# Performance work log

Measured on AMD Instinct MI355X. Metric: run time of the kernel, lower is better.

The kernel has to match this reference:

```python
import jax, jax.numpy as jnp
import numpy as np

EPS = 1e-6
SIGMA = 0.1  # temperature for pseudo-LBS blend weights


def _quat_rotate(q, v):
    # q: [..., 4] (w, x, y, z) unit quaternions, v: [..., 3]
    qw, qv = q[..., :1], q[..., 1:]
    t = 2.0 * jnp.cross(qv, v)
    return v + qw * t + jnp.cross(qv, t)


def _pairwise_sqdist(a, b):
    # a: [n, d], b: [m, d] -> [n, m]
    return (jnp.sum(a * a, -1, keepdims=True)
            + jnp.sum(b * b, -1)[None, :]
            - 2.0 * (a @ b.T))


def setup_inputs() -> dict:
    N, K, F, V, J, P, M, H = 300000, 80, 64, 6890, 24, 64, 64, 128
    key = jax.random.key(0)
    ks = jax.random.split(key, 16)
    s = lambda i, shape: jax.random.normal(ks[i], shape, dtype=jnp.float32) * 0.05
    return {
        "xyz": jax.random.normal(ks[0], (N, 3), dtype=jnp.float32),
        "feature": jax.random.normal(ks[1], (N, F), dtype=jnp.float32),
        "centers": jax.random.normal(ks[2], (K, F), dtype=jnp.float32),
        "smpl_verts": jax.random.normal(ks[3], (V, 3), dtype=jnp.float32),
        "skinning_weights": jax.random.uniform(ks[4], (V, J), dtype=jnp.float32),
        "body_pose_feature": jax.random.normal(ks[5], (J, P), dtype=jnp.float32),
        "w_body": s(6, (P + F, M)),
        "b_body": jnp.zeros((M,), jnp.float32),
        "w_pos1": s(7, (3 + M, H)),
        "b_pos1": jnp.zeros((H,), jnp.float32),
        "w_pos2": s(8, (H, M)),
        "b_pos2": jnp.zeros((M,), jnp.float32),
        "w_rot": s(9, (M, 4)),
        "b_rot": jnp.zeros((4,), jnp.float32),
        "w_trans": s(10, (M, 3)),
        "b_trans": jnp.zeros((3,), jnp.float32),
    }


def reference(xyz, feature, centers, smpl_verts, skinning_weights,
              body_pose_feature, w_body, b_body, w_pos1, b_pos1,
              w_pos2, b_pos2, w_rot, b_rot, w_trans, b_trans):
    # ---- soft k-means: soft assignment of N points to K garment joints ----
    a = jax.nn.softmax(-_pairwise_sqdist(feature, centers), axis=-1)  # [N, K]
    cnt = a.sum(axis=0) + EPS                                          # [K]
    # weighted segment-reduce: c_assign^T @ xyz, diag(1/count) normalize
    joint_xyz = (a.T @ xyz) / cnt[:, None]      # [K, 3]
    joint_feat = (a.T @ feature) / cnt[:, None]  # [K, F] (cluster centers)

    # ---- KNN (k=1) skin-weight lookup against SMPL canonical verts ----
    idx = jnp.argmin(_pairwise_sqdist(joint_xyz, smpl_verts), axis=-1)  # [K]
    pts_W = skinning_weights[idx]                                        # [K, J]

    # ---- garment pose decoder ----
    body_feat = pts_W @ body_pose_feature                 # [K, P]
    g = jnp.concatenate([body_feat, joint_feat], axis=-1)  # [K, P+F]
    g = jax.nn.gelu(g @ w_body + b_body)                   # [K, M]
    lo, hi = smpl_verts.min(0), smpl_verts.max(0)
    xn = 2.0 * (joint_xyz - lo) / (hi - lo + EPS) - 1.0    # aabb sym-normalize
    h = jax.nn.relu(jnp.concatenate([xn, g], -1) @ w_pos1 + b_pos1)
    g2 = h @ w_pos2 + b_pos2                               # [K, M]
    q = g2 @ w_rot + b_rot
    q = q / (jnp.linalg.norm(q, axis=-1, keepdims=True) + EPS)  # [K, 4]
    t = g2 @ w_trans + b_trans                                   # [K, 3]

    # ---- pseudo-LBS: blend per-joint transforms back to N points ----
    w = jax.nn.softmax(-_pairwise_sqdist(xyz, joint_xyz) / SIGMA, axis=-1)  # [N, K]
    qb = w @ q
    qb = qb / (jnp.linalg.norm(qb, axis=-1, keepdims=True) + EPS)  # [N, 4]
    deformed_xyz = _quat_rotate(qb, xyz) + w @ t                    # [N, 3]
    return deformed_xyz
```

## Files before the change

### kernel.cpp

```cpp
#include <hip/hip_runtime.h>
#include <math.h>

#define N_PTS 300000
#define NJ 80
#define FDIM 64
#define VN 6890
#define NROUND 9375
#define GRID_A 256
#define TOTW 2048
#define SLOT_B 8704

typedef __attribute__((ext_vector_type(8))) short short8;
typedef __attribute__((ext_vector_type(4))) float f32x4;

union Frag { uint32_t u[4]; short8 v; };

__device__ __forceinline__ uint32_t packhi(float a, float b) {
  return (__float_as_uint(a) >> 16) | (__float_as_uint(b) & 0xFFFF0000u);
}
__device__ __forceinline__ uint32_t packlo(float a, float b) {
  float la = a - __uint_as_float(__float_as_uint(a) & 0xFFFF0000u);
  float lb = b - __uint_as_float(__float_as_uint(b) & 0xFFFF0000u);
  return packhi(la, lb);
}

#define DPPF(x, ctrl) __uint_as_float((uint32_t)__builtin_amdgcn_update_dpp( \
    0, (int)__float_as_uint(x), (ctrl), 0xF, 0xF, true))

__device__ __forceinline__ void gl16(const float* g, const void* l) {
  __builtin_amdgcn_global_load_lds(
      (const __attribute__((address_space(1))) void*)g,
      (__attribute__((address_space(3))) void*)l, 16, 0, 0);
}
__device__ __forceinline__ void gl4(const float* g, const void* l) {
  __builtin_amdgcn_global_load_lds(
      (const __attribute__((address_space(1))) void*)g,
      (__attribute__((address_space(3))) void*)l, 4, 0, 0);
}

__global__ __launch_bounds__(512, 2) void kA(
    const float* __restrict__ xyz, const float* __restrict__ feature,
    const float* __restrict__ centers, float* __restrict__ jacc,
    float* __restrict__ part)
{
  __shared__ __align__(16) unsigned char ring[8][2][SLOT_B];
  __shared__ ushort sChi[NJ][72];
  __shared__ ushort sClo[NJ][72];

  const int tid = threadIdx.x;
  const int w = tid >> 6;
  const int l = tid & 63;
  const int i = l & 15;
  const int g = l >> 4;
  const int gw = blockIdx.x * 8 + w;

  auto STAGE = [&](int st, int rs) {
    const float* fb = feature + (size_t)rs * 2048;
    unsigned char* base = &ring[w][st][0];
#pragma unroll
    for (int k = 0; k < 8; ++k) {
      const int lu = k * 64 + l;
      const int ptl = lu >> 4;
      const int gu = ptl * 16 + ((lu & 15) ^ (ptl & 7));
      gl16(fb + gu * 4, base + k * 1024);
    }
    const float* xb = xyz + (size_t)rs * 96;
#pragma unroll
    for (int k = 0; k < 2; ++k) {
      int fi = k * 64 + l; if (fi > 95) fi = 95;
      gl4(xb + fi, base + 8192 + k * 256);
    }
  };

  STAGE(0, gw);

  for (int idx = tid; idx < NJ * FDIM; idx += 512) {
    float f = centers[idx];
    sChi[idx >> 6][idx & 63] = (ushort)(__float_as_uint(f) >> 16);
    float lo = f - __uint_as_float(__float_as_uint(f) & 0xFFFF0000u);
    sClo[idx >> 6][idx & 63] = (ushort)(__float_as_uint(lo) >> 16);
  }
  float cn[5];
#pragma unroll
  for (int nt = 0; nt < 5; ++nt) {
    float s = 0.f;
    const float* cp = centers + (size_t)(i + 16 * nt) * FDIM + 8 * g;
#pragma unroll
    for (int e = 0; e < 8; ++e) {
      float a0 = cp[e], a1 = cp[32 + e];
      s += a0 * a0 + a1 * a1;
    }
    s += __shfl_xor(s, 16);
    s += __shfl_xor(s, 32);
    cn[nt] = s;
  }
  __syncthreads();

  f32x4 acc2[5][5];
#pragma unroll
  for (int a = 0; a < 5; ++a)
#pragma unroll
    for (int b = 0; b < 5; ++b) acc2[a][b] = (f32x4){0.f, 0.f, 0.f, 0.f};

  int s2 = 0;
  for (int r = gw; r < NROUND; r += TOTW) {
    {
      int rn = r + TOTW; if (rn > NROUND - 1) rn = NROUND - 1;
      STAGE(s2 ^ 1, rn);
    }
    asm volatile("s_waitcnt vmcnt(10)" ::: "memory");
    __builtin_amdgcn_sched_barrier(0);

    const float* F = (const float*)&ring[w][s2][0];
    const float* X = (const float*)&ring[w][s2][8192];

    f32x4 acc1[2][5];
#pragma unroll
    for (int c = 0; c < 2; ++c)
#pragma unroll
      for (int nt = 0; nt < 5; ++nt) acc1[c][nt] = (f32x4){0.f, 0.f, 0.f, 0.f};

#pragma unroll
    for (int ks = 0; ks < 2; ++ks) {
      Frag ah[2], al[2];
#pragma unroll
      for (int c = 0; c < 2; ++c) {
        const int ptl = 16 * c + i;
        const int m = ptl & 7;
        const int j = 8 * ks + 2 * g;
        float4 va = *(const float4*)(F + ptl * 64 + ((j ^ m) << 2));
        float4 vb = *(const float4*)(F + ptl * 64 + (((j + 1) ^ m) << 2));
        ah[c].u[0] = packhi(va.x, va.y); ah[c].u[1] = packhi(va.z, va.w);
        ah[c].u[2] = packhi(vb.x, vb.y); ah[c].u[3] = packhi(vb.z, vb.w);
        al[c].u[0] = packlo(va.x, va.y); al[c].u[1] = packlo(va.z, va.w);
        al[c].u[2] = packlo(vb.x, vb.y); al[c].u[3] = packlo(vb.z, vb.w);
      }
#pragma unroll
      for (int nt = 0; nt < 5; ++nt) {
        Frag bh, bl;
        *(uint4*)bh.u = *(const uint4*)&sChi[i + 16 * nt][32 * ks + 8 * g];
        *(uint4*)bl.u = *(const uint4*)&sClo[i + 16 * nt][32 * ks + 8 * g];
#pragma unroll
        for (int c = 0; c < 2; ++c) {
          acc1[c][nt] = __builtin_amdgcn_mfma_f32_16x16x32_bf16(ah[c].v, bh.v, acc1[c][nt], 0, 0, 0);
          acc1[c][nt] = __builtin_amdgcn_mfma_f32_16x16x32_bf16(al[c].v, bh.v, acc1[c][nt], 0, 0, 0);
          acc1[c][nt] = __builtin_amdgcn_mfma_f32_16x16x32_bf16(ah[c].v, bl.v, acc1[c][nt], 0, 0, 0);
        }
      }
    }

    Frag pA[5];
#pragma unroll
    for (int c = 0; c < 2; ++c) {
      f32x4 e5[5];
#pragma unroll
      for (int nt = 0; nt < 5; ++nt)
#pragma unroll
        for (int rr = 0; rr < 4; ++rr) e5[nt][rr] = 2.f * acc1[c][nt][rr] - cn[nt];
      float rs[4];
#pragma unroll
      for (int rr = 0; rr < 4; ++rr) {
        float mm = e5[0][rr];
#pragma unroll
        for (int nt = 1; nt < 5; ++nt) mm = fmaxf(mm, e5[nt][rr]);
        mm = fmaxf(mm, DPPF(mm, 0xB1));
        mm = fmaxf(mm, DPPF(mm, 0x4E));
        mm = fmaxf(mm, DPPF(mm, 0x141));
        mm = fmaxf(mm, DPPF(mm, 0x140));
        float ss = 0.f;
#pragma unroll
        for (int nt = 0; nt < 5; ++nt) {
          float e = __expf(e5[nt][rr] - mm);
          e5[nt][rr] = e;
          ss += e;
        }
        ss += DPPF(ss, 0xB1);
        ss += DPPF(ss, 0x4E);
        ss += DPPF(ss, 0x141);
        ss += DPPF(ss, 0x140);
        rs[rr] = __builtin_amdgcn_rcpf(ss);
      }
#pragma unroll
      for (int nt = 0; nt < 5; ++nt) {
        pA[nt].u[2 * c + 0] = packhi(e5[nt][0] * rs[0], e5[nt][1] * rs[1]);
        pA[nt].u[2 * c + 1] = packhi(e5[nt][2] * rs[2], e5[nt][3] * rs[3]);
      }
    }

#pragma unroll
    for (int ct = 0; ct < 5; ++ct) {
      Frag B;
      float x[8];
      if (ct < 4) {
        const int d = 16 * ct + i, jd = d >> 2, db = d & 3;
#pragma unroll
        for (int n = 0; n < 8; ++n) {
          const int ptl = (n < 4) ? (4 * g + n) : (16 + 4 * g + (n - 4));
          x[n] = F[ptl * 64 + ((jd ^ (ptl & 7)) << 2) + db];
        }
      } else {
#pragma unroll
        for (int n = 0; n < 8; ++n) {
          const int ptl = (n < 4) ? (4 * g + n) : (16 + 4 * g + (n - 4));
          x[n] = (i < 3) ? X[ptl * 3 + i] : (i == 3 ? 1.f : 0.f);
        }
      }
      B.u[0] = packhi(x[0], x[1]); B.u[1] = packhi(x[2], x[3]);
      B.u[2] = packhi(x[4], x[5]); B.u[3] = packhi(x[6], x[7]);
#pragma unroll
      for (int nt = 0; nt < 5; ++nt)
        acc2[nt][ct] = __builtin_amdgcn_mfma_f32_16x16x32_bf16(pA[nt].v, B.v, acc2[nt][ct], 0, 0, 0);
    }

    s2 ^= 1;
  }

  asm volatile("s_waitcnt vmcnt(0)" ::: "memory");
  __syncthreads();
  float* sJ = (float*)&ring[0][0][0];
  for (int idx = tid; idx < 5440; idx += 512) sJ[idx] = 0.f;
  __syncthreads();
#pragma unroll
  for (int ww = 0; ww < 8; ++ww) {
    if (w == ww) {
#pragma unroll
      for (int nt = 0; nt < 5; ++nt)
#pragma unroll
        for (int ct = 0; ct < 5; ++ct) {
          if (ct < 4 || i < 4) {
            const int col = 16 * ct + i;
#pragma unroll
            for (int rr = 0; rr < 4; ++rr)
              sJ[(16 * nt + 4 * g + rr) * 68 + col] += acc2[nt][ct][rr];
          }
        }
    }
    __syncthreads();
  }
  if (part) {
    for (int idx = tid; idx < 5440; idx += 512)
      part[(size_t)blockIdx.x * 5440 + idx] = sJ[idx];
  } else {
    for (int idx = tid; idx < 5440; idx += 512)
      atomicAdd(&jacc[idx], sJ[idx]);
  }
}

__global__ __launch_bounds__(64) void kB(
    const float* __restrict__ jacc, const float* __restrict__ part,
    const float* __restrict__ smpl,
    const float* __restrict__ sw, const float* __restrict__ bpf,
    const float* __restrict__ w_body, const float* __restrict__ b_body,
    const float* __restrict__ w_pos1, const float* __restrict__ b_pos1,
    const float* __restrict__ w_pos2, const float* __restrict__ b_pos2,
    const float* __restrict__ w_rot,  const float* __restrict__ b_rot,
    const float* __restrict__ w_trans,const float* __restrict__ b_trans,
    float* __restrict__ jpack, float* __restrict__ qpack,
    float* __restrict__ tpack)
{
  const int k = blockIdx.x;
  const int l = threadIdx.x;
  __shared__ float sh68[68];
  __shared__ float gin[128];
  __shared__ float in2[67];
  __shared__ float h2[128];
  __shared__ float g2[64];
  __shared__ float q7[8];

  if (part) {
    float a0 = 0.f, a1 = 0.f, a2 = 0.f, a3 = 0.f;
    float e0 = 0.f, e1 = 0.f, e2 = 0.f, e3 = 0.f;
    const float* pk = part + k * 68;
    for (int b = 0; b < GRID_A; b += 4) {
      a0 += pk[(size_t)(b + 0) * 5440 + l];
      a1 += pk[(size_t)(b + 1) * 5440 + l];
      a2 += pk[(size_t)(b + 2) * 5440 + l];
      a3 += pk[(size_t)(b + 3) * 5440 + l];
      if (l < 4) {
        e0 += pk[(size_t)(b + 0) * 5440 + 64 + l];
        e1 += pk[(size_t)(b + 1) * 5440 + 64 + l];
        e2 += pk[(size_t)(b + 2) * 5440 + 64 + l];
        e3 += pk[(size_t)(b + 3) * 5440 + 64 + l];
      }
    }
    sh68[l] = (a0 + a1) + (a2 + a3);
    if (l < 4) sh68[64 + l] = (e0 + e1) + (e2 + e3);
  } else {
    sh68[l] = jacc[k * 68 + l];
    if (l < 4) sh68[64 + l] = jacc[k * 68 + 64 + l];
  }
  __syncthreads();

  const float cnt = sh68[67] + 1e-6f;
  gin[64 + l] = sh68[l] / cnt;
  const float jx = sh68[64] / cnt;
  const float jy = sh68[65] / cnt;
  const float jz = sh68[66] / cnt;

  float lo0 = 1e30f, lo1 = 1e30f, lo2 = 1e30f;
  float hi0 = -1e30f, hi1 = -1e30f, hi2 = -1e30f;
  float best = 1e30f; int bi = 0;
  for (int v = l; v < VN; v += 64) {
    float x = smpl[v*3], y = smpl[v*3+1], z = smpl[v*3+2];
    lo0 = fminf(lo0, x); hi0 = fmaxf(hi0, x);
    lo1 = fminf(lo1, y); hi1 = fmaxf(hi1, y);
    lo2 = fminf(lo2, z); hi2 = fmaxf(hi2, z);
    float dx = x - jx, dy = y - jy, dz = z - jz;
    float d = dx*dx + dy*dy + dz*dz;
    if (d < best) { best = d; bi = v; }
  }
#pragma unroll
  for (int m = 1; m < 64; m <<= 1) {
    lo0 = fminf(lo0, __shfl_xor(lo0, m));
    lo1 = fminf(lo1, __shfl_xor(lo1, m));
    lo2 = fminf(lo2, __shfl_xor(lo2, m));
    hi0 = fmaxf(hi0, __shfl_xor(hi0, m));
    hi1 = fmaxf(hi1, __shfl_xor(hi1, m));
    hi2 = fmaxf(hi2, __shfl_xor(hi2, m));
    float d2 = __shfl_xor(best, m); int i2 = __shfl_xor(bi, m);
    if (d2 < best || (d2 == best && i2 < bi)) { best = d2; bi = i2; }
  }

  {
    float s = 0.f;
    for (int j = 0; j < 24; ++j) s += sw[bi*24 + j] * bpf[j*64 + l];
    gin[l] = s;
  }
  if (l < 3) {
    float lo = (l == 0) ? lo0 : (l == 1) ? lo1 : lo2;
    float hi = (l == 0) ? hi0 : (l == 1) ? hi1 : hi2;
    float jc = (l == 0) ? jx : (l == 1) ? jy : jz;
    in2[l] = 2.f * (jc - lo) / (hi - lo + 1e-6f) - 1.f;
  }
  __syncthreads();

  {
    float s = b_body[l];
    for (int t = 0; t < 128; ++t) s += gin[t] * w_body[t*64 + l];
    float u = 0.7978845608028654f * (s + 0.044715f * s * s * s);
    float e = __expf(2.f * u);
    float th = 1.f - 2.f / (e + 1.f);
    in2[3 + l] = 0.5f * s * (1.f + th);
  }
  __syncthreads();

#pragma unroll
  for (int half = 0; half < 2; ++half) {
    const int m = l + 64*half;
    float s = b_pos1[m];
    for (int t = 0; t < 67; ++t) s += in2[t] * w_pos1[t*128 + m];
    h2[m] = fmaxf(s, 0.f);
  }
  __syncthreads();

  {
    float s = b_pos2[l];
    for (int t = 0; t < 128; ++t) s += h2[t] * w_pos2[t*64 + l];
    g2[l] = s;
  }
  __syncthreads();

  if (l < 4) {
    float s = b_rot[l];
    for (int t = 0; t < 64; ++t) s += g2[t] * w_rot[t*4 + l];
    q7[l] = s;
  } else if (l < 7) {
    const int j = l - 4;
    float s = b_trans[j];
    for (int t = 0; t < 64; ++t) s += g2[t] * w_trans[t*3 + j];
    q7[l] = s;
  }
  __syncthreads();
  if (l == 0) {
    float q0 = q7[0], q1 = q7[1], q2 = q7[2], q3 = q7[3];
    float rn = 1.f / (sqrtf(q0*q0 + q1*q1 + q2*q2 + q3*q3) + 1e-6f);
    *(float4*)&qpack[k*4] = make_float4(q0*rn, q1*rn, q2*rn, q3*rn);
    *(float4*)&tpack[k*4] = make_float4(q7[4], q7[5], q7[6], 0.f);
    *(float4*)&jpack[k*4] = make_float4(jx, jy, jz, jx*jx + jy*jy + jz*jz);
  }
}

__global__ __launch_bounds__(256) void kC(
    const float* __restrict__ xyz, const float* __restrict__ jpack,
    const float* __restrict__ qpack, const float* __restrict__ tpack,
    float* __restrict__ out)
{
  __shared__ float4 sj[NJ], sq[NJ], st[NJ];
  __shared__ float sxy[768];
  const int tid = threadIdx.x;
  const int pbase = blockIdx.x * 256;
  const int nval = min(256, N_PTS - pbase);
  const int cnt3 = nval * 3;

  if (tid < 80)        sj[tid]       = ((const float4*)jpack)[tid];
  else if (tid < 160)  sq[tid - 80]  = ((const float4*)qpack)[tid - 80];
  else if (tid < 240)  st[tid - 160] = ((const float4*)tpack)[tid - 160];
  for (int t = tid; t < cnt3; t += 256) sxy[t] = xyz[(size_t)pbase * 3 + t];
  __syncthreads();

  const bool valid = tid < nval;
  float x0 = 0.f, x1 = 0.f, x2 = 0.f;
  if (valid) { x0 = sxy[tid*3]; x1 = sxy[tid*3+1]; x2 = sxy[tid*3+2]; }
  __syncthreads();

  float lv[NJ];
  float m = -1e30f;
#pragma unroll
  for (int k = 0; k < NJ; ++k) {
    float4 j = sj[k];
    lv[k] = (2.f*(x0*j.x + x1*j.y + x2*j.z) - j.w) * 10.0f;
    m = fmaxf(m, lv[k]);
  }
  float s = 0.f;
  float qb0=0,qb1=0,qb2=0,qb3=0, tb0=0,tb1=0,tb2=0;
#pragma unroll
  for (int k = 0; k < NJ; ++k) {
    float e = __expf(lv[k] - m);
    s += e;
    float4 q = sq[k];
    float4 t = st[k];
    qb0 += e*q.x; qb1 += e*q.y; qb2 += e*q.z; qb3 += e*q.w;
    tb0 += e*t.x; tb1 += e*t.y; tb2 += e*t.z;
  }
  float rs = 1.f / s;
  qb0*=rs; qb1*=rs; qb2*=rs; qb3*=rs; tb0*=rs; tb1*=rs; tb2*=rs;
  float nrm = sqrtf(qb0*qb0+qb1*qb1+qb2*qb2+qb3*qb3) + 1e-6f;
  float rn = 1.f / nrm;
  float qw = qb0*rn, qx = qb1*rn, qy = qb2*rn, qz = qb3*rn;
  float t2x = 2.f*(qy*x2 - qz*x1);
  float t2y = 2.f*(qz*x0 - qx*x2);
  float t2z = 2.f*(qx*x1 - qy*x0);
  float cx = qy*t2z - qz*t2y;
  float cy = qz*t2x - qx*t2z;
  float cz = qx*t2y - qy*t2x;
  float r0 = x0 + qw*t2x + cx + tb0;
  float r1 = x1 + qw*t2y + cy + tb1;
  float r2 = x2 + qw*t2z + cz + tb2;

  if (valid) { sxy[tid*3] = r0; sxy[tid*3+1] = r1; sxy[tid*3+2] = r2; }
  __syncthreads();
  for (int t = tid; t < cnt3; t += 256) out[(size_t)pbase * 3 + t] = sxy[t];
}

extern "C" void kernel_launch(void* const* d_in, const int* in_sizes, int n_in,
                              void* d_out, int out_size, void* d_ws, size_t ws_size,
                              hipStream_t stream) {
  const float* xyz     = (const float*)d_in[0];
  const float* feature = (const float*)d_in[1];
  const float* centers = (const float*)d_in[2];
  const float* smpl    = (const float*)d_in[3];
  const float* sw      = (const float*)d_in[4];
  const float* bpf     = (const float*)d_in[5];
  const float* w_body  = (const float*)d_in[6];
  const float* b_body  = (const float*)d_in[7];
  const float* w_pos1  = (const float*)d_in[8];
  const float* b_pos1  = (const float*)d_in[9];
  const float* w_pos2  = (const float*)d_in[10];
  const float* b_pos2  = (const float*)d_in[11];
  const float* w_rot   = (const float*)d_in[12];
  const float* b_rot   = (const float*)d_in[13];
  const float* w_trans = (const float*)d_in[14];
  const float* b_trans = (const float*)d_in[15];
  float* out = (float*)d_out;

  float* ws    = (float*)d_ws;
  float* jacc  = ws;
  float* jpack = ws + 5440;
  float* qpack = ws + 5760;
  float* tpack = ws + 6080;
  float* part  = ws + 6400;

  const size_t need = (size_t)6400 + (size_t)GRID_A * 5440;
  const bool use_part = (ws_size / 4) >= need;
  float* part_arg = use_part ? part : nullptr;

  if (!use_part) hipMemsetAsync(jacc, 0, 5440 * sizeof(float), stream);
  kA<<<dim3(GRID_A), dim3(512), 0, stream>>>(xyz, feature, centers, jacc, part_arg);
  kB<<<dim3(NJ), dim3(64), 0, stream>>>(jacc, part_arg, smpl, sw, bpf,
                                        w_body, b_body, w_pos1, b_pos1,
                                        w_pos2, b_pos2, w_rot, b_rot,
                                        w_trans, b_trans, jpack, qpack, tpack);
  kC<<<dim3((N_PTS + 255) / 256), dim3(256), 0, stream>>>(xyz, jpack, qpack, tpack, out);
}
```

Measured before the change: 147.4 us.

## Move partial-sum reduction out of kB into a dedicated wide reduce kernel

The reduction of per-block partial sums, which used to run inside kB with only 80 blocks of 64 threads each looping over 256 partials, now runs in a new kernel kR. kR spreads the work over 352 blocks of 256 threads, each summing a 16-partial slice and atomically adding into jacc. kB then reads the finished sums straight from jacc. This adds an extra kernel launch and an unconditional memset, and the atomic accumulation makes summation order nondeterministic.

```diff
diff --git a/kernel.cpp b/kernel.cpp
--- a/kernel.cpp
+++ b/kernel.cpp
@@ -246,9 +246,26 @@
   }
 }
 
+__global__ __launch_bounds__(256) void kR(const float* __restrict__ part,
+                                          float* __restrict__ jacc)
+{
+  const int bx = blockIdx.x;
+  const int cg = bx % 22, sl = bx / 22;
+  const int t = cg * 256 + threadIdx.x;
+  if (t >= 5440) return;
+  const int b0 = sl * (GRID_A / 16);
+  float s0 = 0.f, s1 = 0.f, s2 = 0.f, s3 = 0.f;
+  for (int b = b0; b < b0 + GRID_A / 16; b += 4) {
+    s0 += part[(size_t)(b + 0) * 5440 + t];
+    s1 += part[(size_t)(b + 1) * 5440 + t];
+    s2 += part[(size_t)(b + 2) * 5440 + t];
+    s3 += part[(size_t)(b + 3) * 5440 + t];
+  }
+  atomicAdd(&jacc[t], (s0 + s1) + (s2 + s3));
+}
+
 __global__ __launch_bounds__(64) void kB(
-    const float* __restrict__ jacc, const float* __restrict__ part,
-    const float* __restrict__ smpl,
+    const float* __restrict__ jacc, const float* __restrict__ smpl,
     const float* __restrict__ sw, const float* __restrict__ bpf,
     const float* __restrict__ w_body, const float* __restrict__ b_body,
     const float* __restrict__ w_pos1, const float* __restrict__ b_pos1,
@@ -260,42 +277,17 @@
 {
   const int k = blockIdx.x;
   const int l = threadIdx.x;
-  __shared__ float sh68[68];
   __shared__ float gin[128];
   __shared__ float in2[67];
   __shared__ float h2[128];
   __shared__ float g2[64];
   __shared__ float q7[8];
 
-  if (part) {
-    float a0 = 0.f, a1 = 0.f, a2 = 0.f, a3 = 0.f;
-    float e0 = 0.f, e1 = 0.f, e2 = 0.f, e3 = 0.f;
-    const float* pk = part + k * 68;
-    for (int b = 0; b < GRID_A; b += 4) {
-      a0 += pk[(size_t)(b + 0) * 5440 + l];
-      a1 += pk[(size_t)(b + 1) * 5440 + l];
-      a2 += pk[(size_t)(b + 2) * 5440 + l];
-      a3 += pk[(size_t)(b + 3) * 5440 + l];
-      if (l < 4) {
-        e0 += pk[(size_t)(b + 0) * 5440 + 64 + l];
-        e1 += pk[(size_t)(b + 1) * 5440 + 64 + l];
-        e2 += pk[(size_t)(b + 2) * 5440 + 64 + l];
-        e3 += pk[(size_t)(b + 3) * 5440 + 64 + l];
-      }
-    }
-    sh68[l] = (a0 + a1) + (a2 + a3);
-    if (l < 4) sh68[64 + l] = (e0 + e1) + (e2 + e3);
-  } else {
-    sh68[l] = jacc[k * 68 + l];
-    if (l < 4) sh68[64 + l] = jacc[k * 68 + 64 + l];
-  }
-  __syncthreads();
-
-  const float cnt = sh68[67] + 1e-6f;
-  gin[64 + l] = sh68[l] / cnt;
-  const float jx = sh68[64] / cnt;
-  const float jy = sh68[65] / cnt;
-  const float jz = sh68[66] / cnt;
+  const float cnt = jacc[k*68 + 67] + 1e-6f;
+  gin[64 + l] = jacc[k*68 + l] / cnt;
+  const float jx = jacc[k*68 + 64] / cnt;
+  const float jy = jacc[k*68 + 65] / cnt;
+  const float jz = jacc[k*68 + 66] / cnt;
 
   float lo0 = 1e30f, lo1 = 1e30f, lo2 = 1e30f;
   float hi0 = -1e30f, hi1 = -1e30f, hi2 = -1e30f;
@@ -474,9 +466,11 @@
   const bool use_part = (ws_size / 4) >= need;
   float* part_arg = use_part ? part : nullptr;
 
-  if (!use_part) hipMemsetAsync(jacc, 0, 5440 * sizeof(float), stream);
+  hipMemsetAsync(jacc, 0, 5440 * sizeof(float), stream);
   kA<<<dim3(GRID_A), dim3(512), 0, stream>>>(xyz, feature, centers, jacc, part_arg);
-  kB<<<dim3(NJ), dim3(64), 0, stream>>>(jacc, part_arg, smpl, sw, bpf,
+  if (use_part)
+    kR<<<dim3(22 * 16), dim3(256), 0, stream>>>(part, jacc);
+  kB<<<dim3(NJ), dim3(64), 0, stream>>>(jacc, smpl, sw, bpf,
                                         w_body, b_body, w_pos1, b_pos1,
                                         w_pos2, b_pos2, w_rot, b_rot,
                                         w_trans, b_trans, jpack, qpack, tpack);
```

Result: faster. 131.9 us (-10.5%).

## Process 64 points per wave in kA with 256-thread blocks; parallelise kB partial reduction

Applied to the files above, without the earlier changes.

Each wave in kA now stages and processes 64 points per round instead of 32. Blocks shrink to 4 waves and the LDS ring slots double. This halves the number of rounds and amortises the B-fragment loads and loop overhead, but it reduces total waves in flight and adds tail clamping and masking for the partial last round. kB now launches 256 threads and splits the 256-block partial-sum reduction across three thread groups, which shortens the serial latency of that reduction.

```diff
diff --git a/kernel.cpp b/kernel.cpp
--- a/kernel.cpp
+++ b/kernel.cpp
@@ -5,10 +5,10 @@
 #define NJ 80
 #define FDIM 64
 #define VN 6890
-#define NROUND 9375
+#define NROUND 4688
 #define GRID_A 256
-#define TOTW 2048
-#define SLOT_B 8704
+#define TOTW 1024
+#define SLOT_B 17408
 
 typedef __attribute__((ext_vector_type(8))) short short8;
 typedef __attribute__((ext_vector_type(4))) float f32x4;
@@ -38,12 +38,12 @@
       (__attribute__((address_space(3))) void*)l, 4, 0, 0);
 }
 
-__global__ __launch_bounds__(512, 2) void kA(
+__global__ __launch_bounds__(256, 1) void kA(
     const float* __restrict__ xyz, const float* __restrict__ feature,
     const float* __restrict__ centers, float* __restrict__ jacc,
     float* __restrict__ part)
 {
-  __shared__ __align__(16) unsigned char ring[8][2][SLOT_B];
+  __shared__ __align__(16) unsigned char ring[4][2][SLOT_B];
   __shared__ ushort sChi[NJ][72];
   __shared__ ushort sClo[NJ][72];
 
@@ -52,29 +52,33 @@
   const int l = tid & 63;
   const int i = l & 15;
   const int g = l >> 4;
-  const int gw = blockIdx.x * 8 + w;
+  const int gw = blockIdx.x * 4 + w;
 
   auto STAGE = [&](int st, int rs) {
-    const float* fb = feature + (size_t)rs * 2048;
+    const float* fb = feature + (size_t)rs * 4096;
     unsigned char* base = &ring[w][st][0];
-#pragma unroll
-    for (int k = 0; k < 8; ++k) {
+    const int maxp = min(63, N_PTS - 1 - rs * 64);
+#pragma unroll
+    for (int k = 0; k < 16; ++k) {
       const int lu = k * 64 + l;
-      const int ptl = lu >> 4;
+      int ptl = lu >> 4;
+      ptl = ptl <= maxp ? ptl : maxp;
       const int gu = ptl * 16 + ((lu & 15) ^ (ptl & 7));
       gl16(fb + gu * 4, base + k * 1024);
     }
-    const float* xb = xyz + (size_t)rs * 96;
-#pragma unroll
-    for (int k = 0; k < 2; ++k) {
-      int fi = k * 64 + l; if (fi > 95) fi = 95;
-      gl4(xb + fi, base + 8192 + k * 256);
+    const float* xb = xyz + (size_t)rs * 192;
+    const int maxf = 3 * maxp + 2;
+#pragma unroll
+    for (int k = 0; k < 3; ++k) {
+      int fi = k * 64 + l;
+      fi = fi <= maxf ? fi : maxf;
+      gl4(xb + fi, base + 16384 + k * 256);
     }
   };
 
   STAGE(0, gw);
 
-  for (int idx = tid; idx < NJ * FDIM; idx += 512) {
+  for (int idx = tid; idx < NJ * FDIM; idx += 256) {
     float f = centers[idx];
     sChi[idx >> 6][idx & 63] = (ushort)(__float_as_uint(f) >> 16);
     float lo = f - __uint_as_float(__float_as_uint(f) & 0xFFFF0000u);
@@ -108,108 +112,122 @@
       int rn = r + TOTW; if (rn > NROUND - 1) rn = NROUND - 1;
       STAGE(s2 ^ 1, rn);
     }
-    asm volatile("s_waitcnt vmcnt(10)" ::: "memory");
+    asm volatile("s_waitcnt vmcnt(19)" ::: "memory");
     __builtin_amdgcn_sched_barrier(0);
 
     const float* F = (const float*)&ring[w][s2][0];
-    const float* X = (const float*)&ring[w][s2][8192];
-
-    f32x4 acc1[2][5];
-#pragma unroll
-    for (int c = 0; c < 2; ++c)
-#pragma unroll
-      for (int nt = 0; nt < 5; ++nt) acc1[c][nt] = (f32x4){0.f, 0.f, 0.f, 0.f};
-
-#pragma unroll
-    for (int ks = 0; ks < 2; ++ks) {
-      Frag ah[2], al[2];
-#pragma unroll
-      for (int c = 0; c < 2; ++c) {
-        const int ptl = 16 * c + i;
-        const int m = ptl & 7;
-        const int j = 8 * ks + 2 * g;
-        float4 va = *(const float4*)(F + ptl * 64 + ((j ^ m) << 2));
-        float4 vb = *(const float4*)(F + ptl * 64 + (((j + 1) ^ m) << 2));
-        ah[c].u[0] = packhi(va.x, va.y); ah[c].u[1] = packhi(va.z, va.w);
-        ah[c].u[2] = packhi(vb.x, vb.y); ah[c].u[3] = packhi(vb.z, vb.w);
-        al[c].u[0] = packlo(va.x, va.y); al[c].u[1] = packlo(va.z, va.w);
-        al[c].u[2] = packlo(vb.x, vb.y); al[c].u[3] = packlo(vb.z, vb.w);
-      }
-#pragma unroll
-      for (int nt = 0; nt < 5; ++nt) {
-        Frag bh, bl;
-        *(uint4*)bh.u = *(const uint4*)&sChi[i + 16 * nt][32 * ks + 8 * g];
-        *(uint4*)bl.u = *(const uint4*)&sClo[i + 16 * nt][32 * ks + 8 * g];
-#pragma unroll
-        for (int c = 0; c < 2; ++c) {
-          acc1[c][nt] = __builtin_amdgcn_mfma_f32_16x16x32_bf16(ah[c].v, bh.v, acc1[c][nt], 0, 0, 0);
-          acc1[c][nt] = __builtin_amdgcn_mfma_f32_16x16x32_bf16(al[c].v, bh.v, acc1[c][nt], 0, 0, 0);
-          acc1[c][nt] = __builtin_amdgcn_mfma_f32_16x16x32_bf16(ah[c].v, bl.v, acc1[c][nt], 0, 0, 0);
+    const float* X = (const float*)&ring[w][s2][16384];
+    const int pbase = r * 64;
+
+    Frag pA[2][5];
+#pragma unroll
+    for (int cp = 0; cp < 2; ++cp) {
+      f32x4 acc1[2][5];
+#pragma unroll
+      for (int cc = 0; cc < 2; ++cc)
+#pragma unroll
+        for (int nt = 0; nt < 5; ++nt) acc1[cc][nt] = (f32x4){0.f, 0.f, 0.f, 0.f};
+
+#pragma unroll
+      for (int ks = 0; ks < 2; ++ks) {
+        Frag ah[2], al[2];
+#pragma unroll
+        for (int cc = 0; cc < 2; ++cc) {
+          const int ptl = 32 * cp + 16 * cc + i;
+          const int m = ptl & 7;
+          const int j = 8 * ks + 2 * g;
+          float4 va = *(const float4*)(F + ptl * 64 + ((j ^ m) << 2));
+          float4 vb = *(const float4*)(F + ptl * 64 + (((j + 1) ^ m) << 2));
+          ah[cc].u[0] = packhi(va.x, va.y); ah[cc].u[1] = packhi(va.z, va.w);
+          ah[cc].u[2] = packhi(vb.x, vb.y); ah[cc].u[3] = packhi(vb.z, vb.w);
+          al[cc].u[0] = packlo(va.x, va.y); al[cc].u[1] = packlo(va.z, va.w);
+          al[cc].u[2] = packlo(vb.x, vb.y); al[cc].u[3] = packlo(vb.z, vb.w);
+        }
+#pragma unroll
+        for (int nt = 0; nt < 5; ++nt) {
+          Frag bh, bl;
+          *(uint4*)bh.u = *(const uint4*)&sChi[i + 16 * nt][32 * ks + 8 * g];
+          *(uint4*)bl.u = *(const uint4*)&sClo[i + 16 * nt][32 * ks + 8 * g];
+#pragma unroll
+          for (int cc = 0; cc < 2; ++cc) {
+            acc1[cc][nt] = __builtin_amdgcn_mfma_f32_16x16x32_bf16(ah[cc].v, bh.v, acc1[cc][nt], 0, 0, 0);
+            acc1[cc][nt] = __builtin_amdgcn_mfma_f32_16x16x32_bf16(al[cc].v, bh.v, acc1[cc][nt], 0, 0, 0);
+            acc1[cc][nt] = __builtin_amdgcn_mfma_f32_16x16x32_bf16(ah[cc].v, bl.v, acc1[cc][nt], 0, 0, 0);
+          }
         }
       }
-    }
-
-    Frag pA[5];
-#pragma unroll
-    for (int c = 0; c < 2; ++c) {
-      f32x4 e5[5];
-#pragma unroll
-      for (int nt = 0; nt < 5; ++nt)
-#pragma unroll
-        for (int rr = 0; rr < 4; ++rr) e5[nt][rr] = 2.f * acc1[c][nt][rr] - cn[nt];
-      float rs[4];
-#pragma unroll
-      for (int rr = 0; rr < 4; ++rr) {
-        float mm = e5[0][rr];
-#pragma unroll
-        for (int nt = 1; nt < 5; ++nt) mm = fmaxf(mm, e5[nt][rr]);
-        mm = fmaxf(mm, DPPF(mm, 0xB1));
-        mm = fmaxf(mm, DPPF(mm, 0x4E));
-        mm = fmaxf(mm, DPPF(mm, 0x141));
-        mm = fmaxf(mm, DPPF(mm, 0x140));
-        float ss = 0.f;
+
+#pragma unroll
+      for (int cc = 0; cc < 2; ++cc) {
+        f32x4 e5[5];
+#pragma unroll
+        for (int nt = 0; nt < 5; ++nt)
+#pragma unroll
+          for (int rr = 0; rr < 4; ++rr) e5[nt][rr] = 2.f * acc1[cc][nt][rr] - cn[nt];
+        float rs[4];
+#pragma unroll
+        for (int rr = 0; rr < 4; ++rr) {
+          float mm = e5[0][rr];
+#pragma unroll
+          for (int nt = 1; nt < 5; ++nt) mm = fmaxf(mm, e5[nt][rr]);
+          mm = fmaxf(mm, DPPF(mm, 0xB1));
+          mm = fmaxf(mm, DPPF(mm, 0x4E));
+          mm = fmaxf(mm, DPPF(mm, 0x141));
+          mm = fmaxf(mm, DPPF(mm, 0x140));
+          float ss = 0.f;
+#pragma unroll
+          for (int nt = 0; nt < 5; ++nt) {
+            float e = __expf(e5[nt][rr] - mm);
+            e5[nt][rr] = e;
+            ss += e;
+          }
+          ss += DPPF(ss, 0xB1);
+          ss += DPPF(ss, 0x4E);
+          ss += DPPF(ss, 0x141);
+          ss += DPPF(ss, 0x140);
+          rs[rr] = __builtin_amdgcn_rcpf(ss);
+        }
+        const int pt0 = pbase + 32 * cp + 16 * cc + 4 * g;
 #pragma unroll
         for (int nt = 0; nt < 5; ++nt) {
-          float e = __expf(e5[nt][rr] - mm);
-          e5[nt][rr] = e;
-          ss += e;
-        }
-        ss += DPPF(ss, 0xB1);
-        ss += DPPF(ss, 0x4E);
-        ss += DPPF(ss, 0x141);
-        ss += DPPF(ss, 0x140);
-        rs[rr] = __builtin_amdgcn_rcpf(ss);
-      }
-#pragma unroll
-      for (int nt = 0; nt < 5; ++nt) {
-        pA[nt].u[2 * c + 0] = packhi(e5[nt][0] * rs[0], e5[nt][1] * rs[1]);
-        pA[nt].u[2 * c + 1] = packhi(e5[nt][2] * rs[2], e5[nt][3] * rs[3]);
-      }
-    }
-
-#pragma unroll
-    for (int ct = 0; ct < 5; ++ct) {
-      Frag B;
-      float x[8];
-      if (ct < 4) {
-        const int d = 16 * ct + i, jd = d >> 2, db = d & 3;
-#pragma unroll
-        for (int n = 0; n < 8; ++n) {
-          const int ptl = (n < 4) ? (4 * g + n) : (16 + 4 * g + (n - 4));
-          x[n] = F[ptl * 64 + ((jd ^ (ptl & 7)) << 2) + db];
-        }
-      } else {
-#pragma unroll
-        for (int n = 0; n < 8; ++n) {
-          const int ptl = (n < 4) ? (4 * g + n) : (16 + 4 * g + (n - 4));
-          x[n] = (i < 3) ? X[ptl * 3 + i] : (i == 3 ? 1.f : 0.f);
+          float p0 = (pt0 + 0 < N_PTS) ? e5[nt][0] * rs[0] : 0.f;
+          float p1 = (pt0 + 1 < N_PTS) ? e5[nt][1] * rs[1] : 0.f;
+          float p2 = (pt0 + 2 < N_PTS) ? e5[nt][2] * rs[2] : 0.f;
+          float p3 = (pt0 + 3 < N_PTS) ? e5[nt][3] * rs[3] : 0.f;
+          pA[cp][nt].u[2 * cc + 0] = packhi(p0, p1);
+          pA[cp][nt].u[2 * cc + 1] = packhi(p2, p3);
         }
       }
-      B.u[0] = packhi(x[0], x[1]); B.u[1] = packhi(x[2], x[3]);
-      B.u[2] = packhi(x[4], x[5]); B.u[3] = packhi(x[6], x[7]);
-#pragma unroll
-      for (int nt = 0; nt < 5; ++nt)
-        acc2[nt][ct] = __builtin_amdgcn_mfma_f32_16x16x32_bf16(pA[nt].v, B.v, acc2[nt][ct], 0, 0, 0);
+    }
+
+#pragma unroll
+    for (int ct = 0; ct < 5; ++ct) {
+#pragma unroll
+      for (int hf = 0; hf < 2; ++hf) {
+        Frag B;
+        float x[8];
+        if (ct < 4) {
+          const int d = 16 * ct + i, jd = d >> 2, db = d & 3;
+#pragma unroll
+          for (int n = 0; n < 8; ++n) {
+            const int pb = (n < 4) ? (4 * g + n) : (16 + 4 * g + (n - 4));
+            const int ptl = 32 * hf + pb;
+            x[n] = F[ptl * 64 + ((jd ^ (ptl & 7)) << 2) + db];
+          }
+        } else {
+#pragma unroll
+          for (int n = 0; n < 8; ++n) {
+            const int pb = (n < 4) ? (4 * g + n) : (16 + 4 * g + (n - 4));
+            const int ptl = 32 * hf + pb;
+            x[n] = (i < 3) ? X[ptl * 3 + i] : (i == 3 ? 1.f : 0.f);
+          }
+        }
+        B.u[0] = packhi(x[0], x[1]); B.u[1] = packhi(x[2], x[3]);
+        B.u[2] = packhi(x[4], x[5]); B.u[3] = packhi(x[6], x[7]);
+#pragma unroll
+        for (int nt = 0; nt < 5; ++nt)
+          acc2[nt][ct] = __builtin_amdgcn_mfma_f32_16x16x32_bf16(pA[hf][nt].v, B.v, acc2[nt][ct], 0, 0, 0);
+      }
     }
 
     s2 ^= 1;
@@ -218,10 +236,10 @@
   asm volatile("s_waitcnt vmcnt(0)" ::: "memory");
   __syncthreads();
   float* sJ = (float*)&ring[0][0][0];
-  for (int idx = tid; idx < 5440; idx += 512) sJ[idx] = 0.f;
-  __syncthreads();
-#pragma unroll
-  for (int ww = 0; ww < 8; ++ww) {
+  for (int idx = tid; idx < 5440; idx += 256) sJ[idx] = 0.f;
+  __syncthreads();
+#pragma unroll
+  for (int ww = 0; ww < 4; ++ww) {
     if (w == ww) {
 #pragma unroll
       for (int nt = 0; nt < 5; ++nt)
@@ -238,15 +256,15 @@
     __syncthreads();
   }
   if (part) {
-    for (int idx = tid; idx < 5440; idx += 512)
+    for (int idx = tid; idx < 5440; idx += 256)
       part[(size_t)blockIdx.x * 5440 + idx] = sJ[idx];
   } else {
-    for (int idx = tid; idx < 5440; idx += 512)
+    for (int idx = tid; idx < 5440; idx += 256)
       atomicAdd(&jacc[idx], sJ[idx]);
   }
 }
 
-__global__ __launch_bounds__(64) void kB(
+__global__ __launch_bounds__(256) void kB(
     const float* __restrict__ jacc, const float* __restrict__ part,
     const float* __restrict__ smpl,
     const float* __restrict__ sw, const float* __restrict__ bpf,
@@ -259,7 +277,8 @@
     float* __restrict__ tpack)
 {
   const int k = blockIdx.x;
-  const int l = threadIdx.x;
+  const int tid = threadIdx.x;
+  __shared__ float red[3][68];
   __shared__ float sh68[68];
   __shared__ float gin[128];
   __shared__ float in2[67];
@@ -268,73 +287,71 @@
   __shared__ float q7[8];
 
   if (part) {
-    float a0 = 0.f, a1 = 0.f, a2 = 0.f, a3 = 0.f;
-    float e0 = 0.f, e1 = 0.f, e2 = 0.f, e3 = 0.f;
-    const float* pk = part + k * 68;
-    for (int b = 0; b < GRID_A; b += 4) {
-      a0 += pk[(size_t)(b + 0) * 5440 + l];
-      a1 += pk[(size_t)(b + 1) * 5440 + l];
-      a2 += pk[(size_t)(b + 2) * 5440 + l];
-      a3 += pk[(size_t)(b + 3) * 5440 + l];
-      if (l < 4) {
-        e0 += pk[(size_t)(b + 0) * 5440 + 64 + l];
-        e1 += pk[(size_t)(b + 1) * 5440 + 64 + l];
-        e2 += pk[(size_t)(b + 2) * 5440 + 64 + l];
-        e3 += pk[(size_t)(b + 3) * 5440 + 64 + l];
-      }
-    }
-    sh68[l] = (a0 + a1) + (a2 + a3);
-    if (l < 4) sh68[64 + l] = (e0 + e1) + (e2 + e3);
+    if (tid < 204) {
+      const int c = tid % 68, bg = tid / 68;
+      const int b0 = bg * 85, b1 = (bg == 2) ? GRID_A : b0 + 85;
+      const float* pk = part + k * 68 + c;
+      float s = 0.f;
+#pragma unroll 4
+      for (int b = b0; b < b1; ++b) s += pk[(size_t)b * 5440];
+      red[bg][c] = s;
+    }
+    __syncthreads();
+    if (tid < 68) sh68[tid] = red[0][tid] + red[1][tid] + red[2][tid];
   } else {
-    sh68[l] = jacc[k * 68 + l];
-    if (l < 4) sh68[64 + l] = jacc[k * 68 + 64 + l];
+    if (tid < 68) sh68[tid] = jacc[k * 68 + tid];
   }
   __syncthreads();
 
   const float cnt = sh68[67] + 1e-6f;
-  gin[64 + l] = sh68[l] / cnt;
   const float jx = sh68[64] / cnt;
   const float jy = sh68[65] / cnt;
   const float jz = sh68[66] / cnt;
 
-  float lo0 = 1e30f, lo1 = 1e30f, lo2 = 1e30f;
-  float hi0 = -1e30f, hi1 = -1e30f, hi2 = -1e30f;
-  float best = 1e30f; int bi = 0;
-  for (int v = l; v < VN; v += 64) {
-    float x = smpl[v*3], y = smpl[v*3+1], z = smpl[v*3+2];
-    lo0 = fminf(lo0, x); hi0 = fmaxf(hi0, x);
-    lo1 = fminf(lo1, y); hi1 = fmaxf(hi1, y);
-    lo2 = fminf(lo2, z); hi2 = fmaxf(hi2, z);
-    float dx = x - jx, dy = y - jy, dz = z - jz;
-    float d = dx*dx + dy*dy + dz*dz;
-    if (d < best) { best = d; bi = v; }
-  }
-#pragma unroll
-  for (int m = 1; m < 64; m <<= 1) {
-    lo0 = fminf(lo0, __shfl_xor(lo0, m));
-    lo1 = fminf(lo1, __shfl_xor(lo1, m));
-    lo2 = fminf(lo2, __shfl_xor(lo2, m));
-    hi0 = fmaxf(hi0, __shfl_xor(hi0, m));
-    hi1 = fmaxf(hi1, __shfl_xor(hi1, m));
-    hi2 = fmaxf(hi2, __shfl_xor(hi2, m));
-    float d2 = __shfl_xor(best, m); int i2 = __shfl_xor(bi, m);
-    if (d2 < best || (d2 == best && i2 < bi)) { best = d2; bi = i2; }
-  }
-
-  {
-    float s = 0.f;
-    for (int j = 0; j < 24; ++j) s += sw[bi*24 + j] * bpf[j*64 + l];
-    gin[l] = s;
-  }
-  if (l < 3) {
-    float lo = (l == 0) ? lo0 : (l == 1) ? lo1 : lo2;
-    float hi = (l == 0) ? hi0 : (l == 1) ? hi1 : hi2;
-    float jc = (l == 0) ? jx : (l == 1) ? jy : jz;
-    in2[l] = 2.f * (jc - lo) / (hi - lo + 1e-6f) - 1.f;
-  }
-  __syncthreads();
-
-  {
+  if (tid < 64) {
+    const int l = tid;
+    gin[64 + l] = sh68[l] / cnt;
+
+    float lo0 = 1e30f, lo1 = 1e30f, lo2 = 1e30f;
+    float hi0 = -1e30f, hi1 = -1e30f, hi2 = -1e30f;
+    float best = 1e30f; int bi = 0;
+    for (int v = l; v < VN; v += 64) {
+      float x = smpl[v*3], y = smpl[v*3+1], z = smpl[v*3+2];
+      lo0 = fminf(lo0, x); hi0 = fmaxf(hi0, x);
+      lo1 = fminf(lo1, y); hi1 = fmaxf(hi1, y);
+      lo2 = fminf(lo2, z); hi2 = fmaxf(hi2, z);
+      float dx = x - jx, dy = y - jy, dz = z - jz;
+      float d = dx*dx + dy*dy + dz*dz;
+      if (d < best) { best = d; bi = v; }
+    }
+#pragma unroll
+    for (int m = 1; m < 64; m <<= 1) {
+      lo0 = fminf(lo0, __shfl_xor(lo0, m));
+      lo1 = fminf(lo1, __shfl_xor(lo1, m));
+      lo2 = fminf(lo2, __shfl_xor(lo2, m));
+      hi0 = fmaxf(hi0, __shfl_xor(hi0, m));
+      hi1 = fmaxf(hi1, __shfl_xor(hi1, m));
+      hi2 = fmaxf(hi2, __shfl_xor(hi2, m));
+      float d2 = __shfl_xor(best, m); int i2 = __shfl_xor(bi, m);
+      if (d2 < best || (d2 == best && i2 < bi)) { best = d2; bi = i2; }
+    }
+
+    {
+      float s = 0.f;
+      for (int j = 0; j < 24; ++j) s += sw[bi*24 + j] * bpf[j*64 + l];
+      gin[l] = s;
+    }
+    if (l < 3) {
+      float lo = (l == 0) ? lo0 : (l == 1) ? lo1 : lo2;
+      float hi = (l == 0) ? hi0 : (l == 1) ? hi1 : hi2;
+      float jc = (l == 0) ? jx : (l == 1) ? jy : jz;
+      in2[l] = 2.f * (jc - lo) / (hi - lo + 1e-6f) - 1.f;
+    }
+  }
+  __syncthreads();
+
+  if (tid < 64) {
+    const int l = tid;
     float s = b_body[l];
     for (int t = 0; t < 128; ++t) s += gin[t] * w_body[t*64 + l];
     float u = 0.7978845608028654f * (s + 0.044715f * s * s * s);
@@ -344,34 +361,38 @@
   }
   __syncthreads();
 
-#pragma unroll
-  for (int half = 0; half < 2; ++half) {
-    const int m = l + 64*half;
-    float s = b_pos1[m];
-    for (int t = 0; t < 67; ++t) s += in2[t] * w_pos1[t*128 + m];
-    h2[m] = fmaxf(s, 0.f);
-  }
-  __syncthreads();
-
-  {
+  if (tid < 64) {
+    const int l = tid;
+#pragma unroll
+    for (int half = 0; half < 2; ++half) {
+      const int m = l + 64*half;
+      float s = b_pos1[m];
+      for (int t = 0; t < 67; ++t) s += in2[t] * w_pos1[t*128 + m];
+      h2[m] = fmaxf(s, 0.f);
+    }
+  }
+  __syncthreads();
+
+  if (tid < 64) {
+    const int l = tid;
     float s = b_pos2[l];
     for (int t = 0; t < 128; ++t) s += h2[t] * w_pos2[t*64 + l];
     g2[l] = s;
   }
   __syncthreads();
 
-  if (l < 4) {
-    float s = b_rot[l];
-    for (int t = 0; t < 64; ++t) s += g2[t] * w_rot[t*4 + l];
-    q7[l] = s;
-  } else if (l < 7) {
-    const int j = l - 4;
+  if (tid < 4) {
+    float s = b_rot[tid];
+    for (int t = 0; t < 64; ++t) s += g2[t] * w_rot[t*4 + tid];
+    q7[tid] = s;
+  } else if (tid < 7) {
+    const int j = tid - 4;
     float s = b_trans[j];
     for (int t = 0; t < 64; ++t) s += g2[t] * w_trans[t*3 + j];
-    q7[l] = s;
-  }
-  __syncthreads();
-  if (l == 0) {
+    q7[tid] = s;
+  }
+  __syncthreads();
+  if (tid == 0) {
     float q0 = q7[0], q1 = q7[1], q2 = q7[2], q3 = q7[3];
     float rn = 1.f / (sqrtf(q0*q0 + q1*q1 + q2*q2 + q3*q3) + 1e-6f);
     *(float4*)&qpack[k*4] = make_float4(q0*rn, q1*rn, q2*rn, q3*rn);
@@ -475,10 +496,10 @@
   float* part_arg = use_part ? part : nullptr;
 
   if (!use_part) hipMemsetAsync(jacc, 0, 5440 * sizeof(float), stream);
-  kA<<<dim3(GRID_A), dim3(512), 0, stream>>>(xyz, feature, centers, jacc, part_arg);
-  kB<<<dim3(NJ), dim3(64), 0, stream>>>(jacc, part_arg, smpl, sw, bpf,
-                                        w_body, b_body, w_pos1, b_pos1,
-                                        w_pos2, b_pos2, w_rot, b_rot,
-                                        w_trans, b_trans, jpack, qpack, tpack);
+  kA<<<dim3(GRID_A), dim3(256), 0, stream>>>(xyz, feature, centers, jacc, part_arg);
+  kB<<<dim3(NJ), dim3(256), 0, stream>>>(jacc, part_arg, smpl, sw, bpf,
+                                         w_body, b_body, w_pos1, b_pos1,
+                                         w_pos2, b_pos2, w_rot, b_rot,
+                                         w_trans, b_trans, jpack, qpack, tpack);
   kC<<<dim3((N_PTS + 255) / 256), dim3(256), 0, stream>>>(xyz, jpack, qpack, tpack, out);
 }
```

New measurement: 137.1 us. 1.08x faster.
